# Kernel optimization log

Hardware: AMD Instinct MI355X
Metric: run time of the kernel (lower is better)

The kernel has to match this reference:

```python
import jax, jax.numpy as jnp
import numpy as np

B, T, DEMO = 64, 4096, 8
N_MOD, N_POS = 37, 10
D_IN = N_POS + 1 + N_MOD  # 48
PHI_W, LATENT = 128, 128
PSI_W, PSI_L = 128, 128
DOT, HEADS = 64, 4
RHO_W, OUT = 128, 1
MAX_TIME = 1000.0


def _dense_init(key, fan_in, fan_out):
    lim = float(np.sqrt(6.0 / fan_in))  # he_uniform-ish
    return jax.random.uniform(key, (fan_in, fan_out), jnp.float32, -lim, lim)


def setup_inputs() -> dict:
    key = jax.random.key(0)
    ks = jax.random.split(key, 32)
    inp = {}
    inp['demo'] = jax.random.normal(ks[0], (B, DEMO), jnp.float32)
    inp['times'] = jax.random.uniform(ks[1], (B, T, 1), jnp.float32, 0.0, 100.0)
    inp['values'] = jax.random.normal(ks[2], (B, T, 1), jnp.float32)
    inp['measurements'] = jax.random.randint(ks[3], (B, T), 0, N_MOD, jnp.int32)
    # all sequences full length -> N = B*(T+1) static
    inp['segment_ids'] = jnp.repeat(jnp.arange(B, dtype=jnp.int32), T + 1)
    inp['timescales'] = jnp.asarray(MAX_TIME ** np.linspace(0.0, 1.0, N_POS // 2), jnp.float32)
    inp['demo_W1'] = _dense_init(ks[4], DEMO, PHI_W); inp['demo_b1'] = jnp.zeros((PHI_W,), jnp.float32)
    inp['demo_W2'] = _dense_init(ks[5], PHI_W, D_IN); inp['demo_b2'] = jnp.zeros((D_IN,), jnp.float32)
    dims = [D_IN, PHI_W, PHI_W, PHI_W, LATENT]
    for i in range(4):
        inp['phi_W%d' % i] = _dense_init(ks[6 + i], dims[i], dims[i + 1])
        inp['phi_b%d' % i] = jnp.zeros((dims[i + 1],), jnp.float32)
    pdims = [D_IN, PSI_W, PSI_W, PSI_L]
    for i in range(3):
        inp['psi_W%d' % i] = _dense_init(ks[10 + i], pdims[i], pdims[i + 1])
        inp['psi_b%d' % i] = jnp.zeros((pdims[i + 1],), jnp.float32)
    inp['W_k'] = _dense_init(ks[13], PSI_L + D_IN, DOT * HEADS)
    # original inits W_q to zeros (degenerate uniform attention); small random keeps test non-trivial
    inp['W_q'] = jax.random.normal(ks[14], (HEADS, DOT), jnp.float32) * 0.05
    rdims = [LATENT * HEADS, RHO_W, RHO_W, RHO_W, OUT]
    for i in range(4):
        inp['rho_W%d' % i] = _dense_init(ks[15 + i], rdims[i], rdims[i + 1])
        inp['rho_b%d' % i] = jnp.zeros((rdims[i + 1],), jnp.float32)
    return inp


def _forward(demo, times, values, timescales,
             demo_W1, demo_b1, demo_W2, demo_b2,
             phi_W0, phi_b0, phi_W1, phi_b1, phi_W2, phi_b2, phi_W3, phi_b3,
             psi_W0, psi_b0, psi_W1, psi_b1, psi_W2, psi_b2,
             W_k, W_q,
             rho_W0, rho_b0, rho_W1, rho_b1, rho_W2, rho_b2, rho_W3, rho_b3,
             measurements, segment_ids):
    relu = jax.nn.relu
    nseg = demo.shape[0]
    # positional encoding: times [B,T,1] / timescales [5] -> sin|cos -> [B,T,10]
    scaled = times / timescales[None, None, :]
    tt = jnp.concatenate([jnp.sin(scaled), jnp.cos(scaled)], axis=-1)
    meas = jax.nn.one_hot(measurements, N_MOD, dtype=times.dtype)  # [B,T,37]
    combined = jnp.concatenate([tt, values, meas], axis=-1)        # [B,T,48]
    demo_enc = relu(demo @ demo_W1 + demo_b1) @ demo_W2 + demo_b2  # [B,48]
    x = jnp.concatenate([demo_enc[:, None, :], combined], axis=1)  # [B,T+1,48]
    collected = x.reshape(-1, x.shape[-1])                         # [N,48]
    # phi MLP -> encoded [N,LATENT]
    h = collected
    for W, b in ((phi_W0, phi_b0), (phi_W1, phi_b1), (phi_W2, phi_b2), (phi_W3, phi_b3)):
        h = relu(h @ W + b)
    encoded = h
    # psi MLP -> [N,PSI_L], then per-segment mean, scattered back
    p = collected
    for W, b in ((psi_W0, psi_b0), (psi_W1, psi_b1), (psi_W2, psi_b2)):
        p = relu(p @ W + b)
    seg_sum = jax.ops.segment_sum(p, segment_ids, num_segments=nseg)
    counts = jax.ops.segment_sum(jnp.ones((p.shape[0],), p.dtype), segment_ids, num_segments=nseg)
    agg = seg_sum / counts[:, None]
    comb2 = jnp.concatenate([collected, agg[segment_ids]], axis=-1)  # [N, 48+128]
    keys = (comb2 @ W_k).reshape(-1, HEADS, DOT)                     # [N,H,D]
    preattn = jnp.einsum('nhd,hd->nh', keys, W_q) / jnp.sqrt(jnp.float32(DOT))
    # segment softmax per head
    m = jax.ops.segment_max(preattn, segment_ids, num_segments=nseg)
    e = jnp.exp(preattn - m[segment_ids])
    s = jax.ops.segment_sum(e, segment_ids, num_segments=nseg)
    attn = e / s[segment_ids]                                        # [N,H]
    # head-major weighted concat: [N, H*LATENT]
    weighted = (attn[:, :, None] * encoded[:, None, :]).reshape(-1, HEADS * LATENT)
    agg_out = jax.ops.segment_sum(weighted, segment_ids, num_segments=nseg)  # [B,512]
    r = agg_out
    for W, b in ((rho_W0, rho_b0), (rho_W1, rho_b1), (rho_W2, rho_b2)):
        r = relu(r @ W + b)
    return jax.nn.sigmoid(r @ rho_W3 + rho_b3)  # [B,1]


def reference(demo, times, values, timescales,
              demo_W1, demo_b1, demo_W2, demo_b2,
              phi_W0, phi_b0, phi_W1, phi_b1, phi_W2, phi_b2, phi_W3, phi_b3,
              psi_W0, psi_b0, psi_W1, psi_b1, psi_W2, psi_b2,
              W_k, W_q,
              rho_W0, rho_b0, rho_W1, rho_b1, rho_W2, rho_b2, rho_W3, rho_b3,
              measurements, segment_ids):
    return _forward(demo, times, values, timescales,
                    demo_W1, demo_b1, demo_W2, demo_b2,
                    phi_W0, phi_b0, phi_W1, phi_b1, phi_W2, phi_b2, phi_W3, phi_b3,
                    psi_W0, psi_b0, psi_W1, psi_b1, psi_W2, psi_b2,
                    W_k, W_q,
                    rho_W0, rho_b0, rho_W1, rho_b1, rho_W2, rho_b2, rho_W3, rho_b3,
                    measurements, segment_ids)
```

## Files before the change

### kernel.cpp

```cpp
#include <hip/hip_runtime.h>
#include <hip/hip_bf16.h>
#include <math.h>


#define BSEG 64
#define TLEN 4096
#define NPART 9
#define PART_STRIDE 520

#define OFF_DEMO 0
#define OFF_WQ   3072
#define OFF_WT   3264
#define OFF_PARTIALS 31936

typedef __attribute__((ext_vector_type(8))) short short8;
typedef __attribute__((ext_vector_type(4))) float f32x4;

static __device__ __forceinline__ float bfbits2f(unsigned v) { return __uint_as_float(v << 16); }
static __device__ __forceinline__ unsigned short f2bf_rne(float x) {
  unsigned u = __float_as_uint(x);
  unsigned r = (u + 0x7FFFu + ((u >> 16) & 1u)) >> 16;
  return (unsigned short)r;
}
static __device__ __forceinline__ unsigned pk2(float a, float b) {
  float2 f2 = make_float2(a, b);
  __hip_bfloat162 h = __float22bfloat162_rn(f2);
  unsigned u;
  __builtin_memcpy(&u, &h, 4);
  return u;
}

__global__ __launch_bounds__(256) void k_prep(
    const float* __restrict__ demo, const float* __restrict__ dW1, const float* __restrict__ db1,
    const float* __restrict__ dW2, const float* __restrict__ db2,
    const float* __restrict__ Wk, const float* __restrict__ Wq,
    const float* __restrict__ W0, const float* __restrict__ W1,
    const float* __restrict__ W2, const float* __restrict__ W3,
    float* __restrict__ ws) {
  __shared__ float dl[512];
  __shared__ float hd[8192];
  __shared__ float w2[6144];
  int bid = blockIdx.x, tid = threadIdx.x;
  if (bid < 224) {
    unsigned short* wt = (unsigned short*)(ws + OFF_WT);
    int i = bid * 256 + tid;
    float v;
    if (i < 8192) {
      int n = i >> 6, k = i & 63;
      v = (k < 48) ? W0[k * 128 + n] : 0.f;
    } else {
      int j = i - 8192;
      int l = j >> 14, r = j & 16383;
      int n = r >> 7, k = r & 127;
      const float* W = (l == 0) ? W1 : (l == 1) ? W2 : W3;
      v = W[k * 128 + n];
    }
    wt[i] = f2bf_rne(v);
    return;
  }
  if (bid == 224) {
    if (tid < 192) {
      int i = tid >> 2, h = tid & 3;
      float a = 0.f;
      for (int d = 0; d < 64; ++d) a = fmaf(Wk[i * 256 + h * 64 + d], Wq[h * 64 + d], a);
      ws[OFF_WQ + tid] = a * 0.125f;
    }
    return;
  }
  for (int i = tid; i < 512; i += 256) dl[i] = demo[i];
  for (int i = tid; i < 6144; i += 256) w2[i] = dW2[i];
  __syncthreads();
  for (int idx = tid; idx < 8192; idx += 256) {
    int r = idx >> 7, c = idx & 127;
    float a = db1[c];
#pragma unroll
    for (int i = 0; i < 8; ++i) a = fmaf(dl[r * 8 + i], dW1[i * 128 + c], a);
    hd[idx] = fmaxf(a, 0.f);
  }
  __syncthreads();
  for (int idx = tid; idx < 3072; idx += 256) {
    int r = idx / 48, c = idx % 48;
    float a = db2[c];
    for (int k = 0; k < 128; ++k) a = fmaf(hd[r * 128 + k], w2[k * 48 + c], a);
    ws[OFF_DEMO + idx] = a;
  }
}

static __device__ __forceinline__ void mfma_layer(
    const unsigned short* hin, unsigned short* hout,
    const short8 (&Bf)[2][4], const float (&bias)[2],
    int l16, int quad, int n0) {
#pragma unroll
  for (int mt = 0; mt < 4; ++mt) {
    short8 A[4];
#pragma unroll
    for (int s = 0; s < 4; ++s)
      A[s] = *(const short8*)(hin + (mt * 16 + l16) * 136 + s * 32 + quad * 8);
#pragma unroll
    for (int t = 0; t < 2; ++t) {
      f32x4 acc = {bias[t], bias[t], bias[t], bias[t]};
#pragma unroll
      for (int s = 0; s < 4; ++s)
        acc = __builtin_amdgcn_mfma_f32_16x16x32_bf16(A[s], Bf[t][s], acc, 0, 0, 0);
      int col = n0 + t * 16 + l16;
      int base = (mt * 16 + quad * 4) * 136 + col;
      unsigned u01 = pk2(fmaxf(acc[0], 0.f), fmaxf(acc[1], 0.f));
      unsigned u23 = pk2(fmaxf(acc[2], 0.f), fmaxf(acc[3], 0.f));
      hout[base]           = (unsigned short)u01;
      hout[base + 136]     = (unsigned short)(u01 >> 16);
      hout[base + 2 * 136] = (unsigned short)u23;
      hout[base + 3 * 136] = (unsigned short)(u23 >> 16);
    }
  }
}
static __device__ __forceinline__ void mfma_layer0(
    const unsigned short* cin, unsigned short* hout,
    const short8 (&B0)[2][2], const float (&bias0)[2],
    int l16, int quad, int n0) {
#pragma unroll
  for (int mt = 0; mt < 4; ++mt) {
    short8 A0[2];
#pragma unroll
    for (int s = 0; s < 2; ++s)
      A0[s] = *(const short8*)(cin + (mt * 16 + l16) * 72 + s * 32 + quad * 8);
#pragma unroll
    for (int t = 0; t < 2; ++t) {
      f32x4 acc = {bias0[t], bias0[t], bias0[t], bias0[t]};
      acc = __builtin_amdgcn_mfma_f32_16x16x32_bf16(A0[0], B0[t][0], acc, 0, 0, 0);
      acc = __builtin_amdgcn_mfma_f32_16x16x32_bf16(A0[1], B0[t][1], acc, 0, 0, 0);
      int col = n0 + t * 16 + l16;
      int base = (mt * 16 + quad * 4) * 136 + col;
      unsigned u01 = pk2(fmaxf(acc[0], 0.f), fmaxf(acc[1], 0.f));
      unsigned u23 = pk2(fmaxf(acc[2], 0.f), fmaxf(acc[3], 0.f));
      hout[base]           = (unsigned short)u01;
      hout[base + 136]     = (unsigned short)(u01 >> 16);
      hout[base + 2 * 136] = (unsigned short)u23;
      hout[base + 3 * 136] = (unsigned short)(u23 >> 16);
    }
  }
}

__global__ __launch_bounds__(256, 2) void k_main(
    const float* __restrict__ times, const float* __restrict__ values,
    const int* __restrict__ meas, const float* __restrict__ tsc,
    const float* __restrict__ ws,
    const float* __restrict__ b0g, const float* __restrict__ b1g,
    const float* __restrict__ b2g, const float* __restrict__ b3g,
    float* __restrict__ part) {
  __shared__ __align__(16) unsigned short hA[64 * 136];
  __shared__ __align__(16) unsigned short hB[64 * 136];
  __shared__ __align__(16) float preb[512 * 4];
  __shared__ float wql[192];
  __shared__ float mred[16];
  __shared__ float mblk[4];
  int tid = threadIdx.x;
  const int lane = tid & 63, wv = tid >> 6, quad = lane >> 4, l16 = lane & 15;
  const int n0 = wv * 32;

  const unsigned short* wt = (const unsigned short*)(ws + OFF_WT);
  short8 B0[2][2], B1[2][4], B2[2][4], B3[2][4];
  float bias0[2], bias1[2], bias2[2], bias3[2];
#pragma unroll
  for (int t = 0; t < 2; ++t) {
    int n = n0 + t * 16 + l16;
    bias0[t] = b0g[n]; bias1[t] = b1g[n]; bias2[t] = b2g[n]; bias3[t] = b3g[n];
#pragma unroll
    for (int s = 0; s < 2; ++s)
      B0[t][s] = *(const short8*)(wt + n * 64 + s * 32 + quad * 8);
#pragma unroll
    for (int s = 0; s < 4; ++s) {
      B1[t][s] = *(const short8*)(wt + 8192  + n * 128 + s * 32 + quad * 8);
      B2[t][s] = *(const short8*)(wt + 24576 + n * 128 + s * 32 + quad * 8);
      B3[t][s] = *(const short8*)(wt + 40960 + n * 128 + s * 32 + quad * 8);
    }
  }
  if (tid < 192) wql[tid] = ws[OFF_WQ + tid];
  __syncthreads();

  if (blockIdx.x == 512) {
    {
      int r = tid >> 2, cs = tid & 3;
      unsigned short seg[16];
#pragma unroll
      for (int i = 0; i < 16; ++i) seg[i] = 0;
      if (cs < 3)
#pragma unroll
        for (int i = 0; i < 16; ++i) seg[i] = f2bf_rne(ws[OFF_DEMO + r * 48 + cs * 16 + i]);
      unsigned u[8];
#pragma unroll
      for (int i = 0; i < 8; ++i) u[i] = (unsigned)seg[2 * i] | ((unsigned)seg[2 * i + 1] << 16);
      uint4* dst = (uint4*)(hB + r * 72 + cs * 16);
      dst[0] = make_uint4(u[0], u[1], u[2], u[3]);
      dst[1] = make_uint4(u[4], u[5], u[6], u[7]);
    }
    float pre;
    {
      int r = tid >> 2, h = tid & 3;
      float a = 0.f;
      for (int i = 0; i < 48; ++i) a = fmaf(ws[OFF_DEMO + r * 48 + i], wql[i * 4 + h], a);
      pre = a;
    }
    __syncthreads();
    mfma_layer0(hB, hA, B0, bias0, l16, quad, n0); __syncthreads();
    mfma_layer(hA, hB, B1, bias1, l16, quad, n0); __syncthreads();
    mfma_layer(hB, hA, B2, bias2, l16, quad, n0); __syncthreads();
    mfma_layer(hA, hB, B3, bias3, l16, quad, n0); __syncthreads();
    {
      int r = tid >> 2, h = tid & 3;
      float* P = part + (r * NPART + 8) * PART_STRIDE;
      P[h] = pre;
      P[4 + h] = 1.f;
    }
    for (int i = tid; i < 64 * 512; i += 256) {
      int r = i >> 9, rem = i & 511, l = rem & 127;
      part[(r * NPART + 8) * PART_STRIDE + 8 + rem] = bfbits2f(hB[r * 136 + l]);
    }
    return;
  }

  int b = blockIdx.x >> 3, c = blockIdx.x & 7;
  int t0 = c << 9;
  float invts[5];
#pragma unroll
  for (int i = 0; i < 5; ++i) invts[i] = 1.f / tsc[i];

  float mloc[4] = {-1e30f, -1e30f, -1e30f, -1e30f};
  for (int rr = 0; rr < 2; ++rr) {
    int r = tid + rr * 256;
    int t = t0 + r;
    float tv = times[b * TLEN + t];
    float vvv = values[b * TLEN + t];
    int mm = meas[b * TLEN + t];
    float f[11];
#pragma unroll
    for (int i = 0; i < 5; ++i) { float s = tv * invts[i]; f[i] = __sinf(s); f[5 + i] = __cosf(s); }
    f[10] = vvv;
#pragma unroll
    for (int h = 0; h < 4; ++h) {
      float a = wql[(11 + mm) * 4 + h];
#pragma unroll
      for (int i = 0; i < 11; ++i) a = fmaf(f[i], wql[i * 4 + h], a);
      preb[r * 4 + h] = a;
      mloc[h] = fmaxf(mloc[h], a);
    }
  }
#pragma unroll
  for (int off = 32; off > 0; off >>= 1)
#pragma unroll
    for (int h = 0; h < 4; ++h) mloc[h] = fmaxf(mloc[h], __shfl_xor(mloc[h], off, 64));
  if (lane == 0)
#pragma unroll
    for (int h = 0; h < 4; ++h) mred[wv * 4 + h] = mloc[h];
  __syncthreads();
  if (tid < 4)
    mblk[tid] = fmaxf(fmaxf(mred[tid], mred[4 + tid]), fmaxf(mred[8 + tid], mred[12 + tid]));
  __syncthreads();
  for (int i = tid; i < 2048; i += 256) preb[i] = __expf(preb[i] - mblk[i & 3]);
  __syncthreads();

  float pacc[2][4] = {{0.f, 0.f, 0.f, 0.f}, {0.f, 0.f, 0.f, 0.f}};
  for (int tile = 0; tile < 8; ++tile) {
    int rb = tile << 6;
    {
      int r = tid >> 2, cs = tid & 3;
      int t = t0 + rb + r;
      unsigned short seg[16];
#pragma unroll
      for (int i = 0; i < 16; ++i) seg[i] = 0;
      if (cs == 0) {
        float tv = times[b * TLEN + t];
        float vvv = values[b * TLEN + t];
#pragma unroll
        for (int i = 0; i < 5; ++i) {
          float s = tv * invts[i];
          seg[i] = f2bf_rne(__sinf(s));
          seg[5 + i] = f2bf_rne(__cosf(s));
        }
        seg[10] = f2bf_rne(vvv);
      }
      int kk = 11 + meas[b * TLEN + t];
      if ((kk >> 4) == cs) seg[kk & 15] = 0x3F80;
      unsigned u[8];
#pragma unroll
      for (int i = 0; i < 8; ++i) u[i] = (unsigned)seg[2 * i] | ((unsigned)seg[2 * i + 1] << 16);
      uint4* dst = (uint4*)(hB + r * 72 + cs * 16);
      dst[0] = make_uint4(u[0], u[1], u[2], u[3]);
      dst[1] = make_uint4(u[4], u[5], u[6], u[7]);
    }
    __syncthreads();
    mfma_layer0(hB, hA, B0, bias0, l16, quad, n0); __syncthreads();
    mfma_layer(hA, hB, B1, bias1, l16, quad, n0); __syncthreads();
    mfma_layer(hB, hA, B2, bias2, l16, quad, n0); __syncthreads();
#pragma unroll
    for (int mt = 0; mt < 4; ++mt) {
      short8 A[4];
#pragma unroll
      for (int s = 0; s < 4; ++s)
        A[s] = *(const short8*)(hA + (mt * 16 + l16) * 136 + s * 32 + quad * 8);
      f32x4 acc0 = {bias3[0], bias3[0], bias3[0], bias3[0]};
      f32x4 acc1 = {bias3[1], bias3[1], bias3[1], bias3[1]};
#pragma unroll
      for (int s = 0; s < 4; ++s) {
        acc0 = __builtin_amdgcn_mfma_f32_16x16x32_bf16(A[s], B3[0][s], acc0, 0, 0, 0);
        acc1 = __builtin_amdgcn_mfma_f32_16x16x32_bf16(A[s], B3[1][s], acc1, 0, 0, 0);
      }
#pragma unroll
      for (int j = 0; j < 4; ++j) {
        int row = rb + mt * 16 + quad * 4 + j;
        float4 e4 = *(const float4*)(preb + row * 4);
        float v0 = fmaxf(acc0[j], 0.f), v1 = fmaxf(acc1[j], 0.f);
        pacc[0][0] = fmaf(v0, e4.x, pacc[0][0]);
        pacc[0][1] = fmaf(v0, e4.y, pacc[0][1]);
        pacc[0][2] = fmaf(v0, e4.z, pacc[0][2]);
        pacc[0][3] = fmaf(v0, e4.w, pacc[0][3]);
        pacc[1][0] = fmaf(v1, e4.x, pacc[1][0]);
        pacc[1][1] = fmaf(v1, e4.y, pacc[1][1]);
        pacc[1][2] = fmaf(v1, e4.z, pacc[1][2]);
        pacc[1][3] = fmaf(v1, e4.w, pacc[1][3]);
      }
    }
    __syncthreads();
  }
#pragma unroll
  for (int t = 0; t < 2; ++t)
#pragma unroll
    for (int h = 0; h < 4; ++h) {
      float v = pacc[t][h];
      v += __shfl_xor(v, 16, 64);
      v += __shfl_xor(v, 32, 64);
      pacc[t][h] = v;
    }
  float* P = part + (b * NPART + c) * PART_STRIDE;
  if (tid < 4) P[tid] = mblk[tid];
  {
    float s4[4];
#pragma unroll
    for (int h = 0; h < 4; ++h) s4[h] = preb[tid * 4 + h] + preb[(tid + 256) * 4 + h];
#pragma unroll
    for (int off = 32; off > 0; off >>= 1)
#pragma unroll
      for (int h = 0; h < 4; ++h) s4[h] += __shfl_xor(s4[h], off, 64);
    if (lane == 0)
#pragma unroll
      for (int h = 0; h < 4; ++h) mred[wv * 4 + h] = s4[h];
    __syncthreads();
    if (tid < 4) P[4 + tid] = mred[tid] + mred[4 + tid] + mred[8 + tid] + mred[12 + tid];
  }
  if (quad == 0)
#pragma unroll
    for (int t = 0; t < 2; ++t)
#pragma unroll
      for (int h = 0; h < 4; ++h)
        P[8 + h * 128 + (n0 + t * 16 + l16)] = pacc[t][h];
}

__global__ __launch_bounds__(256) void k_combine(
    const float* __restrict__ part,
    const float* __restrict__ rW0, const float* __restrict__ rb0,
    const float* __restrict__ rW1, const float* __restrict__ rb1,
    const float* __restrict__ rW2, const float* __restrict__ rb2,
    const float* __restrict__ rW3, const float* __restrict__ rb3,
    float* __restrict__ out) {
  __shared__ float mg[4], Ss[4], sc[36], agg[512], r1[128], p0[256];
  int tid = threadIdx.x;
  int b = blockIdx.x;
  const float* P = part + b * NPART * PART_STRIDE;
  if (tid < 4) {
    float m = -1e30f;
    for (int p = 0; p < NPART; ++p) m = fmaxf(m, P[p * PART_STRIDE + tid]);
    mg[tid] = m;
  }
  __syncthreads();
  if (tid < 36) {
    int p = tid >> 2, h = tid & 3;
    sc[tid] = __expf(P[p * PART_STRIDE + h] - mg[h]);
  }
  __syncthreads();
  if (tid < 4) {
    float s = 0.f;
    for (int p = 0; p < NPART; ++p) s += P[p * PART_STRIDE + 4 + tid] * sc[p * 4 + tid];
    Ss[tid] = s;
  }
  __syncthreads();
  for (int idx = tid; idx < 512; idx += 256) {
    int h = idx >> 7;
    float a = 0.f;
    for (int p = 0; p < NPART; ++p) a = fmaf(P[p * PART_STRIDE + 8 + idx], sc[p * 4 + h], a);
    agg[idx] = a / Ss[h];
  }
  __syncthreads();
  const int col = tid & 127, half = tid >> 7;
  {
    float a = 0.f;
    for (int k = half * 256; k < half * 256 + 256; ++k) a = fmaf(agg[k], rW0[k * 128 + col], a);
    p0[tid] = a;
  }
  __syncthreads();
  if (tid < 128) r1[tid] = fmaxf(rb0[tid] + p0[tid] + p0[128 + tid], 0.f);
  __syncthreads();
  {
    float a = 0.f;
    for (int k = half * 64; k < half * 64 + 64; ++k) a = fmaf(r1[k], rW1[k * 128 + col], a);
    p0[tid] = a;
  }
  __syncthreads();
  if (tid < 128) r1[tid] = fmaxf(rb1[tid] + p0[tid] + p0[128 + tid], 0.f);
  __syncthreads();
  {
    float a = 0.f;
    for (int k = half * 64; k < half * 64 + 64; ++k) a = fmaf(r1[k], rW2[k * 128 + col], a);
    p0[tid] = a;
  }
  __syncthreads();
  if (tid < 128) p0[tid] = fmaxf(rb2[tid] + p0[tid] + p0[128 + tid], 0.f) * rW3[tid];
  __syncthreads();
  if (tid == 0) {
    float a = rb3[0];
    for (int k = 0; k < 128; ++k) a += p0[k];
    out[b] = 1.f / (1.f + __expf(-a));
  }
}

extern "C" void kernel_launch(void* const* d_in, const int* in_sizes, int n_in,
                              void* d_out, int out_size, void* d_ws, size_t ws_size,
                              hipStream_t stream) {
  const float* demo   = (const float*)d_in[0];
  const float* times  = (const float*)d_in[1];
  const float* values = (const float*)d_in[2];
  const int*   meas   = (const int*)d_in[3];
  const float* tsc = (const float*)d_in[5];
  const float* dW1 = (const float*)d_in[6];
  const float* db1 = (const float*)d_in[7];
  const float* dW2 = (const float*)d_in[8];
  const float* db2 = (const float*)d_in[9];
  const float* pW0 = (const float*)d_in[10];
  const float* pb0 = (const float*)d_in[11];
  const float* pW1 = (const float*)d_in[12];
  const float* pb1 = (const float*)d_in[13];
  const float* pW2 = (const float*)d_in[14];
  const float* pb2 = (const float*)d_in[15];
  const float* pW3 = (const float*)d_in[16];
  const float* pb3 = (const float*)d_in[17];
  const float* Wk  = (const float*)d_in[24];
  const float* Wq  = (const float*)d_in[25];
  const float* rW0 = (const float*)d_in[26];
  const float* rb0 = (const float*)d_in[27];
  const float* rW1 = (const float*)d_in[28];
  const float* rb1 = (const float*)d_in[29];
  const float* rW2 = (const float*)d_in[30];
  const float* rb2 = (const float*)d_in[31];
  const float* rW3 = (const float*)d_in[32];
  const float* rb3 = (const float*)d_in[33];
  float* ws = (float*)d_ws;
  float* partials = ws + OFF_PARTIALS;

  k_prep<<<226, 256, 0, stream>>>(demo, dW1, db1, dW2, db2, Wk, Wq,
                                  pW0, pW1, pW2, pW3, ws);
  k_main<<<513, 256, 0, stream>>>(times, values, meas, tsc, ws,
                                  pb0, pb1, pb2, pb3, partials);
  k_combine<<<64, 256, 0, stream>>>(partials, rW0, rb0, rW1, rb1, rW2, rb2, rW3, rb3,
                                    (float*)d_out);
}
```

Baseline: 198.0 us.

## Fuse combine into main kernel via atomic accumulation and last-block completion

Removes the separate combine kernel. Each block now atomically adds its unnormalised exp-weighted sums into a per-segment accumulator, and a per-segment counter picks the last-arriving block to run the rho MLP and write the output. The max-subtraction for softmax stability is dropped, since without a shared max the raw exps can be summed directly. This saves a kernel launch and the partials round trip. The cost is float atomic contention, a serial combine tail inside the last block, no overflow protection on exp, and non-deterministic summation order.

Result: slower. 217.9 us (+10.0%).

```diff
diff --git a/kernel.cpp b/kernel.cpp
--- a/kernel.cpp
+++ b/kernel.cpp
@@ -6,12 +6,14 @@
 #define BSEG 64
 #define TLEN 4096
 #define NPART 9
-#define PART_STRIDE 520
+#define AGG_STRIDE 520
 
 #define OFF_DEMO 0
 #define OFF_WQ   3072
 #define OFF_WT   3264
-#define OFF_PARTIALS 31936
+#define OFF_AGG  31936
+#define OFF_CNT  65216
+#define ZERO_SPAN 33344
 
 typedef __attribute__((ext_vector_type(8))) short short8;
 typedef __attribute__((ext_vector_type(4))) float f32x4;
@@ -65,6 +67,7 @@
       for (int d = 0; d < 64; ++d) a = fmaf(Wk[i * 256 + h * 64 + d], Wq[h * 64 + d], a);
       ws[OFF_WQ + tid] = a * 0.125f;
     }
+    for (int i = tid; i < ZERO_SPAN; i += 256) ws[OFF_AGG + i] = 0.f;
     return;
   }
   for (int i = tid; i < 512; i += 256) dl[i] = demo[i];
@@ -140,22 +143,78 @@
   }
 }
 
+static __device__ __forceinline__ void seg_combine(
+    int b, float* cw, float* aggf,
+    const float* __restrict__ rW0, const float* __restrict__ rb0,
+    const float* __restrict__ rW1, const float* __restrict__ rb1,
+    const float* __restrict__ rW2, const float* __restrict__ rb2,
+    const float* __restrict__ rW3, const float* __restrict__ rb3,
+    float* __restrict__ out, int tid) {
+  float* agg = cw;
+  float* r1  = cw + 512;
+  float* p0  = cw + 640;
+  float* raw = cw + 1024;
+  float* A = aggf + b * AGG_STRIDE;
+  __syncthreads();
+  for (int idx = tid; idx < 516; idx += 256) raw[idx] = atomicAdd(A + idx, 0.f);
+  __syncthreads();
+  for (int idx = tid; idx < 512; idx += 256) agg[idx] = raw[4 + idx] / raw[idx >> 7];
+  __syncthreads();
+  const int col = tid & 127, half = tid >> 7;
+  {
+    float a = 0.f;
+    for (int k = half * 256; k < half * 256 + 256; ++k) a = fmaf(agg[k], rW0[k * 128 + col], a);
+    p0[tid] = a;
+  }
+  __syncthreads();
+  if (tid < 128) r1[tid] = fmaxf(rb0[tid] + p0[tid] + p0[128 + tid], 0.f);
+  __syncthreads();
+  {
+    float a = 0.f;
+    for (int k = half * 64; k < half * 64 + 64; ++k) a = fmaf(r1[k], rW1[k * 128 + col], a);
+    p0[tid] = a;
+  }
+  __syncthreads();
+  if (tid < 128) r1[tid] = fmaxf(rb1[tid] + p0[tid] + p0[128 + tid], 0.f);
+  __syncthreads();
+  {
+    float a = 0.f;
+    for (int k = half * 64; k < half * 64 + 64; ++k) a = fmaf(r1[k], rW2[k * 128 + col], a);
+    p0[tid] = a;
+  }
+  __syncthreads();
+  if (tid < 128) p0[tid] = fmaxf(rb2[tid] + p0[tid] + p0[128 + tid], 0.f) * rW3[tid];
+  __syncthreads();
+  if (tid == 0) {
+    float a = rb3[0];
+    for (int k = 0; k < 128; ++k) a += p0[k];
+    out[b] = 1.f / (1.f + __expf(-a));
+  }
+}
+
 __global__ __launch_bounds__(256, 2) void k_main(
     const float* __restrict__ times, const float* __restrict__ values,
     const int* __restrict__ meas, const float* __restrict__ tsc,
-    const float* __restrict__ ws,
+    float* __restrict__ ws,
     const float* __restrict__ b0g, const float* __restrict__ b1g,
     const float* __restrict__ b2g, const float* __restrict__ b3g,
-    float* __restrict__ part) {
+    const float* __restrict__ rW0, const float* __restrict__ rb0,
+    const float* __restrict__ rW1, const float* __restrict__ rb1,
+    const float* __restrict__ rW2, const float* __restrict__ rb2,
+    const float* __restrict__ rW3, const float* __restrict__ rb3,
+    float* __restrict__ out) {
   __shared__ __align__(16) unsigned short hA[64 * 136];
   __shared__ __align__(16) unsigned short hB[64 * 136];
-  __shared__ __align__(16) float preb[512 * 4];
+  __shared__ __align__(16) float preb[2048];
   __shared__ float wql[192];
   __shared__ float mred[16];
-  __shared__ float mblk[4];
+  __shared__ float sblk[4];
+  __shared__ int winflag[64];
   int tid = threadIdx.x;
   const int lane = tid & 63, wv = tid >> 6, quad = lane >> 4, l16 = lane & 15;
   const int n0 = wv * 32;
+  float* aggf = ws + OFF_AGG;
+  int* cnt = (int*)ws + OFF_CNT;
 
   const unsigned short* wt = (const unsigned short*)(ws + OFF_WT);
   short8 B0[2][2], B1[2][4], B2[2][4], B3[2][4];
@@ -177,7 +236,7 @@
   if (tid < 192) wql[tid] = ws[OFF_WQ + tid];
   __syncthreads();
 
-  if (blockIdx.x == 512) {
+  if (blockIdx.x == 0) {
     {
       int r = tid >> 2, cs = tid & 3;
       unsigned short seg[16];
@@ -193,38 +252,41 @@
       dst[0] = make_uint4(u[0], u[1], u[2], u[3]);
       dst[1] = make_uint4(u[4], u[5], u[6], u[7]);
     }
-    float pre;
     {
       int r = tid >> 2, h = tid & 3;
       float a = 0.f;
       for (int i = 0; i < 48; ++i) a = fmaf(ws[OFF_DEMO + r * 48 + i], wql[i * 4 + h], a);
-      pre = a;
+      float e = __expf(a);
+      preb[tid] = e;
+      atomicAdd(aggf + r * AGG_STRIDE + h, e);
     }
     __syncthreads();
     mfma_layer0(hB, hA, B0, bias0, l16, quad, n0); __syncthreads();
     mfma_layer(hA, hB, B1, bias1, l16, quad, n0); __syncthreads();
     mfma_layer(hB, hA, B2, bias2, l16, quad, n0); __syncthreads();
     mfma_layer(hA, hB, B3, bias3, l16, quad, n0); __syncthreads();
-    {
-      int r = tid >> 2, h = tid & 3;
-      float* P = part + (r * NPART + 8) * PART_STRIDE;
-      P[h] = pre;
-      P[4 + h] = 1.f;
-    }
     for (int i = tid; i < 64 * 512; i += 256) {
-      int r = i >> 9, rem = i & 511, l = rem & 127;
-      part[(r * NPART + 8) * PART_STRIDE + 8 + rem] = bfbits2f(hB[r * 136 + l]);
-    }
+      int r = i >> 9, rem = i & 511;
+      int h = rem >> 7, l = rem & 127;
+      atomicAdd(aggf + r * AGG_STRIDE + 4 + rem, preb[r * 4 + h] * bfbits2f(hB[r * 136 + l]));
+    }
+    __syncthreads();
+    if (tid < BSEG) winflag[tid] = (atomicAdd(cnt + tid, 1) == NPART - 1) ? 1 : 0;
+    __syncthreads();
+    for (int s = 0; s < BSEG; ++s)
+      if (winflag[s])
+        seg_combine(s, preb, aggf, rW0, rb0, rW1, rb1, rW2, rb2, rW3, rb3, out, tid);
     return;
   }
 
-  int b = blockIdx.x >> 3, c = blockIdx.x & 7;
+  int bx = blockIdx.x - 1;
+  int b = bx >> 3, c = bx & 7;
   int t0 = c << 9;
   float invts[5];
 #pragma unroll
   for (int i = 0; i < 5; ++i) invts[i] = 1.f / tsc[i];
 
-  float mloc[4] = {-1e30f, -1e30f, -1e30f, -1e30f};
+  float s4[4] = {0.f, 0.f, 0.f, 0.f};
   for (int rr = 0; rr < 2; ++rr) {
     int r = tid + rr * 256;
     int t = t0 + r;
@@ -240,23 +302,20 @@
       float a = wql[(11 + mm) * 4 + h];
 #pragma unroll
       for (int i = 0; i < 11; ++i) a = fmaf(f[i], wql[i * 4 + h], a);
-      preb[r * 4 + h] = a;
-      mloc[h] = fmaxf(mloc[h], a);
+      float e = __expf(a);
+      preb[r * 4 + h] = e;
+      s4[h] += e;
     }
   }
 #pragma unroll
   for (int off = 32; off > 0; off >>= 1)
 #pragma unroll
-    for (int h = 0; h < 4; ++h) mloc[h] = fmaxf(mloc[h], __shfl_xor(mloc[h], off, 64));
+    for (int h = 0; h < 4; ++h) s4[h] += __shfl_xor(s4[h], off, 64);
   if (lane == 0)
 #pragma unroll
-    for (int h = 0; h < 4; ++h) mred[wv * 4 + h] = mloc[h];
-  __syncthreads();
-  if (tid < 4)
-    mblk[tid] = fmaxf(fmaxf(mred[tid], mred[4 + tid]), fmaxf(mred[8 + tid], mred[12 + tid]));
-  __syncthreads();
-  for (int i = tid; i < 2048; i += 256) preb[i] = __expf(preb[i] - mblk[i & 3]);
-  __syncthreads();
+    for (int h = 0; h < 4; ++h) mred[wv * 4 + h] = s4[h];
+  __syncthreads();
+  if (tid < 4) sblk[tid] = mred[tid] + mred[4 + tid] + mred[8 + tid] + mred[12 + tid];
 
   float pacc[2][4] = {{0.f, 0.f, 0.f, 0.f}, {0.f, 0.f, 0.f, 0.f}};
   for (int tile = 0; tile < 8; ++tile) {
@@ -330,95 +389,19 @@
       v += __shfl_xor(v, 32, 64);
       pacc[t][h] = v;
     }
-  float* P = part + (b * NPART + c) * PART_STRIDE;
-  if (tid < 4) P[tid] = mblk[tid];
-  {
-    float s4[4];
-#pragma unroll
-    for (int h = 0; h < 4; ++h) s4[h] = preb[tid * 4 + h] + preb[(tid + 256) * 4 + h];
-#pragma unroll
-    for (int off = 32; off > 0; off >>= 1)
-#pragma unroll
-      for (int h = 0; h < 4; ++h) s4[h] += __shfl_xor(s4[h], off, 64);
-    if (lane == 0)
-#pragma unroll
-      for (int h = 0; h < 4; ++h) mred[wv * 4 + h] = s4[h];
-    __syncthreads();
-    if (tid < 4) P[4 + tid] = mred[tid] + mred[4 + tid] + mred[8 + tid] + mred[12 + tid];
-  }
+  float* A = aggf + b * AGG_STRIDE;
+  if (tid < 4) atomicAdd(A + tid, sblk[tid]);
   if (quad == 0)
 #pragma unroll
     for (int t = 0; t < 2; ++t)
 #pragma unroll
       for (int h = 0; h < 4; ++h)
-        P[8 + h * 128 + (n0 + t * 16 + l16)] = pacc[t][h];
-}
-
-__global__ __launch_bounds__(256) void k_combine(
-    const float* __restrict__ part,
-    const float* __restrict__ rW0, const float* __restrict__ rb0,
-    const float* __restrict__ rW1, const float* __restrict__ rb1,
-    const float* __restrict__ rW2, const float* __restrict__ rb2,
-    const float* __restrict__ rW3, const float* __restrict__ rb3,
-    float* __restrict__ out) {
-  __shared__ float mg[4], Ss[4], sc[36], agg[512], r1[128], p0[256];
-  int tid = threadIdx.x;
-  int b = blockIdx.x;
-  const float* P = part + b * NPART * PART_STRIDE;
-  if (tid < 4) {
-    float m = -1e30f;
-    for (int p = 0; p < NPART; ++p) m = fmaxf(m, P[p * PART_STRIDE + tid]);
-    mg[tid] = m;
-  }
-  __syncthreads();
-  if (tid < 36) {
-    int p = tid >> 2, h = tid & 3;
-    sc[tid] = __expf(P[p * PART_STRIDE + h] - mg[h]);
-  }
-  __syncthreads();
-  if (tid < 4) {
-    float s = 0.f;
-    for (int p = 0; p < NPART; ++p) s += P[p * PART_STRIDE + 4 + tid] * sc[p * 4 + tid];
-    Ss[tid] = s;
-  }
-  __syncthreads();
-  for (int idx = tid; idx < 512; idx += 256) {
-    int h = idx >> 7;
-    float a = 0.f;
-    for (int p = 0; p < NPART; ++p) a = fmaf(P[p * PART_STRIDE + 8 + idx], sc[p * 4 + h], a);
-    agg[idx] = a / Ss[h];
-  }
-  __syncthreads();
-  const int col = tid & 127, half = tid >> 7;
-  {
-    float a = 0.f;
-    for (int k = half * 256; k < half * 256 + 256; ++k) a = fmaf(agg[k], rW0[k * 128 + col], a);
-    p0[tid] = a;
-  }
-  __syncthreads();
-  if (tid < 128) r1[tid] = fmaxf(rb0[tid] + p0[tid] + p0[128 + tid], 0.f);
-  __syncthreads();
-  {
-    float a = 0.f;
-    for (int k = half * 64; k < half * 64 + 64; ++k) a = fmaf(r1[k], rW1[k * 128 + col], a);
-    p0[tid] = a;
-  }
-  __syncthreads();
-  if (tid < 128) r1[tid] = fmaxf(rb1[tid] + p0[tid] + p0[128 + tid], 0.f);
-  __syncthreads();
-  {
-    float a = 0.f;
-    for (int k = half * 64; k < half * 64 + 64; ++k) a = fmaf(r1[k], rW2[k * 128 + col], a);
-    p0[tid] = a;
-  }
-  __syncthreads();
-  if (tid < 128) p0[tid] = fmaxf(rb2[tid] + p0[tid] + p0[128 + tid], 0.f) * rW3[tid];
-  __syncthreads();
-  if (tid == 0) {
-    float a = rb3[0];
-    for (int k = 0; k < 128; ++k) a += p0[k];
-    out[b] = 1.f / (1.f + __expf(-a));
-  }
+        atomicAdd(A + 4 + h * 128 + (n0 + t * 16 + l16), pacc[t][h]);
+  __syncthreads();
+  if (tid == 0) winflag[0] = (atomicAdd(cnt + b, 1) == NPART - 1) ? 1 : 0;
+  __syncthreads();
+  if (winflag[0])
+    seg_combine(b, preb, aggf, rW0, rb0, rW1, rb1, rW2, rb2, rW3, rb3, out, tid);
 }
 
 extern "C" void kernel_launch(void* const* d_in, const int* in_sizes, int n_in,
@@ -452,12 +435,11 @@
   const float* rW3 = (const float*)d_in[32];
   const float* rb3 = (const float*)d_in[33];
   float* ws = (float*)d_ws;
-  float* partials = ws + OFF_PARTIALS;
 
   k_prep<<<226, 256, 0, stream>>>(demo, dW1, db1, dW2, db2, Wk, Wq,
                                   pW0, pW1, pW2, pW3, ws);
   k_main<<<513, 256, 0, stream>>>(times, values, meas, tsc, ws,
-                                  pb0, pb1, pb2, pb3, partials);
-  k_combine<<<64, 256, 0, stream>>>(partials, rW0, rb0, rW1, rb1, rW2, rb2, rW3, rb3,
-                                    (float*)d_out);
-}
+                                  pb0, pb1, pb2, pb3,
+                                  rW0, rb0, rW1, rb1, rW2, rb2, rW3, rb3,
+                                  (float*)d_out);
+}
```
